# Kernel tuning notes

Hardware: AMD Instinct MI355X
Metric: run time of the kernel (lower is better)

Reference implementation:

```python
import jax, jax.numpy as jnp
import numpy as np

B, D, H, K = 16384, 128, 1024, 8
OPD = 3 * K + 1  # params per dim
TB = 3.0         # tail_bound: left=bottom=-TB, right=top=TB
EPS = 1e-12
MIN_W = MIN_H = MIN_D = 1e-3


def _masks():
    rng = np.random.RandomState(0)
    in_deg = np.arange(1, D + 1)
    h1 = rng.randint(1, D, size=(H,))
    h2 = rng.randint(1, D, size=(H,))
    out_deg = np.arange(1, D + 1)
    m1 = (in_deg[None, :] <= h1[:, None]).astype(np.float32)          # [H, D]
    m2 = (h1[None, :] <= h2[:, None]).astype(np.float32)              # [H, H]
    m3 = np.repeat((out_deg[:, None] > h2[None, :]).astype(np.float32), OPD, axis=0)  # [D*OPD, H]
    return jnp.asarray(m1), jnp.asarray(m2), jnp.asarray(m3)


def _kaiming(key, fan_out, fan_in, a=0.1):
    bound = np.sqrt(6.0 / ((1.0 + a * a) * fan_in))
    return jax.random.uniform(key, (fan_out, fan_in), jnp.float32, -bound, bound)


def setup_inputs() -> dict:
    key = jax.random.key(0)
    kx, k1, k2, k3 = jax.random.split(key, 4)
    m1, m2, m3 = _masks()
    return {
        'x': jax.random.normal(kx, (B, D), jnp.float32),
        'W1': _kaiming(k1, H, D), 'b1': jnp.zeros((H,), jnp.float32),
        'W2': _kaiming(k2, H, H), 'b2': jnp.zeros((H,), jnp.float32),
        'W3': _kaiming(k3, D * OPD, H), 'b3': jnp.zeros((D * OPD,), jnp.float32),
        'm1': m1, 'm2': m2, 'm3': m3,
    }


def _norm_cum(u, mn):
    k = u.shape[-1]
    w = jax.nn.softmax(u, axis=-1)
    w = mn + (1.0 - mn * k) * w
    c = jnp.cumsum(w, axis=-1)
    c = jnp.pad(c, [(0, 0)] * (c.ndim - 1) + [(1, 0)])
    c = c / jnp.clip(c[..., -1:], 1e-12)
    return c[..., 1:] - c[..., :-1], c


def _take(p, idx):
    return jnp.take_along_axis(p, idx[..., None], axis=-1)[..., 0]


def _forward(x, W1, b1, W2, b2, W3, b3, m1, m2, m3):
    h = jax.nn.silu(x @ (W1 * m1).T + b1)
    h = jax.nn.silu(h @ (W2 * m2).T + b2)
    raw = (h @ (W3 * m3).T + b3).reshape(-1, D, OPD)  # [B, D, 3K+1]
    uw, uh, ud = raw[..., :K], raw[..., K:2 * K], raw[..., 2 * K:]
    w, cw = _norm_cum(uw, MIN_W)
    hh, ch = _norm_cum(uh, MIN_H)
    d = MIN_D + jax.nn.softplus(ud)  # [B, D, K+1]

    left, right, bottom, top = -TB, TB, -TB, TB
    inside = (x >= left) & (x <= right)  # [B, D]
    xs = jnp.clip((x - left) / (right - left), 0.0, 1.0)
    bid = jnp.clip(jnp.sum((xs[..., None] >= cw), axis=-1) - 1, 0, K - 1)
    xk, wk = _take(cw, bid), _take(w, bid)
    yk, hk = _take(ch, bid), _take(hh, bid)
    dk, dk1 = _take(d, bid), _take(d, bid + 1)
    t = jnp.clip((xs - xk) / (wk + EPS), 0.0, 1.0)
    a = (hk + EPS) / (wk + EPS)
    num = a * t * t + dk * t * (1 - t)
    den = a + (dk + dk1 - 2 * a) * t * (1 - t)
    s = num / (den + EPS)
    y = (yk + hk * s) * (top - bottom) + bottom
    dnum = a * a * (dk1 * t * t + 2 * a * t * (1 - t) + dk * (1 - t) * (1 - t))
    dydx = (top - bottom) / (right - left) * dnum / (den * den + EPS)
    out = jnp.where(inside, y, x)
    lad = jnp.where(inside, jnp.log(jnp.clip(dydx, 1e-12)), 0.0)
    return out, jnp.sum(lad, axis=-1)


def reference(x, W1, b1, W2, b2, W3, b3, m1, m2, m3):
    return _forward(x, W1, b1, W2, b2, W3, b3, m1, m2, m3)
```

## Files before the change

### kernel.cpp

```cpp
#include <hip/hip_runtime.h>
#include <hip/hip_bf16.h>

#define BATCH 16384
#define DIM   128
#define HID   1024
#define NK    8
#define OPD   25
#define N3    (DIM*OPD)
#define NP    3328

typedef __attribute__((ext_vector_type(8))) short  short8;
typedef __attribute__((ext_vector_type(4))) float  floatx4;
typedef unsigned int u32;

__device__ __forceinline__ float fexp(float x) { return __expf(x); }
__device__ __forceinline__ float flog(float x) { return __logf(x); }
__device__ __forceinline__ float fdiv(float a, float b) { return __fdividef(a, b); }

__device__ __forceinline__ void async_copy16(const unsigned short* g,
                                             unsigned short* l) {
    __builtin_amdgcn_global_load_lds(
        (const __attribute__((address_space(1))) u32*)g,
        (__attribute__((address_space(3))) u32*)l,
        16, 0, 0);
}

__device__ __forceinline__ void swizzle_bid(int bid, int NT,
                                            int& tile, int& m) {
    const int xcd  = bid & 7;
    const int u    = bid >> 3;
    const int ph   = NT * 8;
    const int half = u / ph;
    const int rem  = u % ph;
    const int trank = rem >> 3;
    const int msub  = rem & 7;
    tile = NT - 1 - trank;
    m    = xcd * 16 + half * 8 + msub;
}

__global__ __launch_bounds__(128) void hsum_kernel(
    const float* __restrict__ m1, const float* __restrict__ m3,
    int* __restrict__ h1i, int* __restrict__ h2i) {
    const int b = blockIdx.x, t = threadIdx.x;
    if (b < HID) {
        float v = m1[b * DIM + t];
        #pragma unroll
        for (int off = 32; off > 0; off >>= 1) v += __shfl_down(v, off, 64);
        __shared__ float ws[2];
        if ((t & 63) == 0) ws[t >> 6] = v;
        __syncthreads();
        if (t == 0) h1i[b] = (int)(ws[0] + ws[1] + 0.5f);
    } else {
        const int j = (b - HID) * 128 + t;
        float s = 0.f;
        for (int d = 0; d < DIM; d++) s += m3[(size_t)d * OPD * HID + j];
        h2i[j] = DIM - (int)(s + 0.5f);
    }
}

__global__ __launch_bounds__(1024) void sort_kernel(
    const int* __restrict__ h1i, const int* __restrict__ h2i,
    int* __restrict__ perm1, int* __restrict__ perm2,
    int* __restrict__ h1sv, int* __restrict__ h2sv,
    int* __restrict__ klim1, int* __restrict__ klim2, int* __restrict__ klim3)
{
    __shared__ int hist[128];
    __shared__ int h1s[1024], h2s[1024];
    const int t = threadIdx.x;
    const int h1v = h1i[t], h2v = h2i[t];

    if (t < 128) hist[t] = 0;
    __syncthreads();
    atomicAdd(&hist[h1v], 1);
    __syncthreads();
    if (t == 0) { int a = 0; for (int b = 0; b < 128; b++) { int c = hist[b]; hist[b] = a; a += c; } }
    __syncthreads();
    int r = atomicAdd(&hist[h1v], 1);
    perm1[r] = t; h1s[r] = h1v; h1sv[r] = h1v;
    __syncthreads();
    if (t < 128) hist[t] = 0;
    __syncthreads();
    atomicAdd(&hist[h2v], 1);
    __syncthreads();
    if (t == 0) { int a = 0; for (int b = 0; b < 128; b++) { int c = hist[b]; hist[b] = a; a += c; } }
    __syncthreads();
    r = atomicAdd(&hist[h2v], 1);
    perm2[r] = t; h2s[r] = h2v; h2sv[r] = h2v;
    __syncthreads();

    if (t < 8) {
        klim1[t] = ((h1s[t * 128 + 127] + 63) >> 6) << 6;
        int mh = h2s[t * 128 + 127];
        int c = 0;
        for (int j = 0; j < 1024; j++) c += (h1s[j] <= mh) ? 1 : 0;
        klim2[t] = ((c + 63) >> 6) << 6;
    }
    if (t < 26) {
        int dmax = t * 5 + 4; if (dmax > 127) dmax = 127;
        int c = 0;
        for (int j = 0; j < 1024; j++) c += (h2s[j] <= dmax) ? 1 : 0;
        klim3[t] = ((c + 63) >> 6) << 6;
    }
}

__global__ __launch_bounds__(256) void wperm_kernel(
    const float* __restrict__ W1, const float* __restrict__ b1,
    const float* __restrict__ W2, const float* __restrict__ b2,
    const float* __restrict__ W3, const float* __restrict__ x,
    const int* __restrict__ perm1, const int* __restrict__ perm2,
    const int* __restrict__ h1sv, const int* __restrict__ h2sv,
    __hip_bfloat16* __restrict__ w1p, float* __restrict__ b1p,
    __hip_bfloat16* __restrict__ w2p, float* __restrict__ b2p,
    __hip_bfloat16* __restrict__ w3p,
    __hip_bfloat16* __restrict__ xb, float* __restrict__ lad)
{
    __shared__ float row[HID];
    const int b = blockIdx.x, t = threadIdx.x;
    if (b < 512) {
        const int i = b * 256 + t;
        const int hp = i >> 7, col = i & 127;
        const int src = perm1[hp];
        float v = (col < h1sv[hp]) ? W1[src * DIM + col] : 0.f;
        w1p[i] = __float2bfloat16(v);
        if (col == 0) b1p[hp] = b1[src];
    } else if (b < 512 + HID) {
        const int ip = b - 512;
        const int si = perm2[ip];
        const int h2v = h2sv[ip];
        #pragma unroll
        for (int q = 0; q < 4; q++) row[q * 256 + t] = W2[(size_t)si * HID + q * 256 + t];
        __syncthreads();
        #pragma unroll
        for (int q = 0; q < 4; q++) {
            const int jp = q * 256 + t;
            float v = (h1sv[jp] <= h2v) ? row[perm1[jp]] : 0.f;
            w2p[(size_t)ip * HID + jp] = __float2bfloat16(v);
        }
        if (t == 0) b2p[ip] = b2[si];
    } else if (b < 512 + HID + NP) {
        const int c = b - 512 - HID;
        const int s = c & 127, t3 = c >> 7;
        if (s >= 125) {
            #pragma unroll
            for (int q = 0; q < 4; q++)
                w3p[(size_t)c * HID + q * 256 + t] = __float2bfloat16(0.f);
            return;
        }
        const int srcrow = t3 * 125 + s;
        const int d = srcrow / 25;
        #pragma unroll
        for (int q = 0; q < 4; q++) row[q * 256 + t] = W3[(size_t)srcrow * HID + q * 256 + t];
        __syncthreads();
        #pragma unroll
        for (int q = 0; q < 4; q++) {
            const int kk = q * 256 + t;
            float v = (h2sv[kk] <= d) ? row[perm2[kk]] : 0.f;
            w3p[(size_t)c * HID + kk] = __float2bfloat16(v);
        }
    } else {
        const int i = (b - (512 + HID + NP)) * 256 + t;
        xb[i] = __float2bfloat16(x[i]);
        if (i < BATCH) lad[i] = 0.f;
    }
}

__device__ __forceinline__ void spline_eval(const float* __restrict__ p,
                                            float xv, float& yout, float& lout) {
    float cw[NK + 1], ch[NK + 1];
    {
        float mx = p[0];
        #pragma unroll
        for (int j = 1; j < NK; j++) mx = fmaxf(mx, p[j]);
        float e[NK], s = 0.f;
        #pragma unroll
        for (int j = 0; j < NK; j++) { e[j] = fexp(p[j] - mx); s += e[j]; }
        const float inv = fdiv(1.f, s);
        cw[0] = 0.f;
        #pragma unroll
        for (int j = 0; j < NK; j++) cw[j + 1] = cw[j] + (0.001f + 0.992f * e[j] * inv);
    }
    {
        float mx = p[8];
        #pragma unroll
        for (int j = 1; j < NK; j++) mx = fmaxf(mx, p[8 + j]);
        float e[NK], s = 0.f;
        #pragma unroll
        for (int j = 0; j < NK; j++) { e[j] = fexp(p[8 + j] - mx); s += e[j]; }
        const float inv = fdiv(1.f, s);
        ch[0] = 0.f;
        #pragma unroll
        for (int j = 0; j < NK; j++) ch[j + 1] = ch[j] + (0.001f + 0.992f * e[j] * inv);
    }
    const float icw = fdiv(1.f, fmaxf(cw[NK], 1e-12f));
    const float ich = fdiv(1.f, fmaxf(ch[NK], 1e-12f));

    const bool inside = (xv >= -3.f) && (xv <= 3.f);
    float xs = (xv + 3.f) * (1.f / 6.f);
    xs = fminf(fmaxf(xs, 0.f), 1.f);
    const float xsc = xs * cw[NK];

    float xk = 0.f, wk = cw[1], yk = 0.f, hk = ch[1];
    float uda = p[16], udb = p[17];
    #pragma unroll
    for (int j = 1; j < NK; j++) {
        const bool c = (xsc >= cw[j]);
        xk  = c ? cw[j] : xk;
        wk  = c ? (cw[j + 1] - cw[j]) : wk;
        yk  = c ? ch[j] : yk;
        hk  = c ? (ch[j + 1] - ch[j]) : hk;
        uda = c ? p[16 + j] : uda;
        udb = c ? p[17 + j] : udb;
    }
    xk *= icw; wk *= icw;
    yk *= ich; hk *= ich;

    const float dk  = 0.001f + ((uda > 20.f) ? uda : flog(1.f + fexp(uda)));
    const float dk1 = 0.001f + ((udb > 20.f) ? udb : flog(1.f + fexp(udb)));

    float t = fdiv(xs - xk, wk + 1e-12f);
    t = fminf(fmaxf(t, 0.f), 1.f);
    const float a   = fdiv(hk + 1e-12f, wk + 1e-12f);
    const float omt = 1.f - t;
    const float tt1 = t * omt;
    const float num = a * t * t + dk * tt1;
    const float den = a + (dk + dk1 - 2.f * a) * tt1;
    const float s   = fdiv(num, den + 1e-12f);
    const float y   = (yk + hk * s) * 6.f - 3.f;
    const float dnum = a * a * (dk1 * t * t + 2.f * a * tt1 + dk * omt * omt);
    const float dydx = fdiv(dnum, den * den + 1e-12f);

    yout = inside ? y : xv;
    lout = inside ? flog(fmaxf(dydx, 1e-12f)) : 0.f;
}

__global__ __launch_bounds__(256, 4) void gemm_bt_kernel(
    const unsigned short* __restrict__ A,
    const unsigned short* __restrict__ Bw,
    const float* __restrict__ bias,
    const int* __restrict__ klim,
    __hip_bfloat16* __restrict__ Cout,
    int M, int N, int Kd)
{
    constexpr int BM = 128, BN = 128, BK = 64;
    __shared__ unsigned short As[BM * BK];
    __shared__ unsigned short Bs[BN * BK];

    const int bid = blockIdx.y * gridDim.x + blockIdx.x;
    int tile, mpan;
    swizzle_bid(bid, gridDim.x, tile, mpan);
    const int bn = tile * BN;
    const int bm = mpan * BM;
    const int Klim = klim[tile];

    const int t    = threadIdx.x;
    const int lane = t & 63;
    const int w    = t >> 6;
    const int wr   = (w >> 1) * 64;
    const int wc   = (w & 1) * 64;
    const int lr   = lane & 15;
    const int quad = lane >> 4;
    const int lxor = lr & 7;

    floatx4 acc[4][4] = {};

    const int lrow = lane >> 3;
    const int lcol = ((lane & 7) ^ lrow) * 8;

    for (int k0 = 0; k0 < Klim; k0 += BK) {
        __syncthreads();
        #pragma unroll
        for (int p = 0; p < 4; p++) {
            const int q = w * 4 + p;
            const int r = q * 8 + lrow;
            async_copy16(&A[(size_t)(bm + r) * Kd + k0 + lcol],
                         &As[q * 512 + lane * 8]);
            async_copy16(&Bw[(size_t)(bn + r) * Kd + k0 + lcol],
                         &Bs[q * 512 + lane * 8]);
        }
        __syncthreads();
        #pragma unroll
        for (int ks = 0; ks < BK; ks += 32) {
            const int cbase = (ks >> 3) + quad;
            const int coff  = (cbase ^ lxor) * 8;
            short8 af[4], bfr[4];
            #pragma unroll
            for (int i = 0; i < 4; i++)
                af[i] = *(const short8*)&As[(wr + i * 16 + lr) * BK + coff];
            #pragma unroll
            for (int j = 0; j < 4; j++)
                bfr[j] = *(const short8*)&Bs[(wc + j * 16 + lr) * BK + coff];
            #pragma unroll
            for (int i = 0; i < 4; i++)
                #pragma unroll
                for (int j = 0; j < 4; j++)
                    acc[i][j] = __builtin_amdgcn_mfma_f32_16x16x32_bf16(
                        af[i], bfr[j], acc[i][j], 0, 0, 0);
        }
    }

    #pragma unroll
    for (int j = 0; j < 4; j++) {
        const int col = bn + wc + j * 16 + lr;
        const float bv = bias[col];
        #pragma unroll
        for (int i = 0; i < 4; i++) {
            const int rowb = bm + wr + i * 16 + quad * 4;
            #pragma unroll
            for (int r = 0; r < 4; r++) {
                float v = acc[i][j][r] + bv;
                v = v * fdiv(1.f, 1.f + fexp(-v));
                Cout[(size_t)(rowb + r) * N + col] = __float2bfloat16(v);
            }
        }
    }
}

__global__ __launch_bounds__(256, 4) void gemm3_spline_kernel(
    const unsigned short* __restrict__ A,
    const unsigned short* __restrict__ Bw,
    const float* __restrict__ b3,
    const int* __restrict__ klim,
    const float* __restrict__ x,
    float* __restrict__ out,
    float* __restrict__ lad,
    int M)
{
    constexpr int BM = 128, BN = 128, BK = 64, Kd = HID;
    constexpr int GS = 28;
    constexpr int RS = 140;
    __shared__ __align__(16) char smem[64 * RS * 4 + 128 * 4];
    unsigned short* As = (unsigned short*)smem;
    unsigned short* Bs = (unsigned short*)(smem + BM * BK * 2);
    float* eb     = (float*)smem;
    float* ladacc = (float*)(smem + 64 * RS * 4);

    const int bid = blockIdx.y * gridDim.x + blockIdx.x;
    int tile, mpan;
    swizzle_bid(bid, gridDim.x, tile, mpan);
    const int bn = tile * BN;
    const int bm = mpan * BM;
    const int Klim = klim[tile];

    const int t    = threadIdx.x;
    const int lane = t & 63;
    const int w    = t >> 6;
    const int wr   = (w >> 1) * 64;
    const int wc   = (w & 1) * 64;
    const int lr   = lane & 15;
    const int quad = lane >> 4;
    const int lxor = lr & 7;

    if (t < 128) ladacc[t] = 0.f;

    floatx4 acc[4][4] = {};

    const int lrow = lane >> 3;
    const int lcol = ((lane & 7) ^ lrow) * 8;

    for (int k0 = 0; k0 < Klim; k0 += BK) {
        __syncthreads();
        #pragma unroll
        for (int p = 0; p < 4; p++) {
            const int q = w * 4 + p;
            const int r = q * 8 + lrow;
            async_copy16(&A[(size_t)(bm + r) * Kd + k0 + lcol],
                         &As[q * 512 + lane * 8]);
            async_copy16(&Bw[(size_t)(bn + r) * Kd + k0 + lcol],
                         &Bs[q * 512 + lane * 8]);
        }
        __syncthreads();
        #pragma unroll
        for (int ks = 0; ks < BK; ks += 32) {
            const int cbase = (ks >> 3) + quad;
            const int coff  = (cbase ^ lxor) * 8;
            short8 af[4], bfr[4];
            #pragma unroll
            for (int i = 0; i < 4; i++)
                af[i] = *(const short8*)&As[(wr + i * 16 + lr) * BK + coff];
            #pragma unroll
            for (int j = 0; j < 4; j++)
                bfr[j] = *(const short8*)&Bs[(wc + j * 16 + lr) * BK + coff];
            #pragma unroll
            for (int i = 0; i < 4; i++)
                #pragma unroll
                for (int j = 0; j < 4; j++)
                    acc[i][j] = __builtin_amdgcn_mfma_f32_16x16x32_bf16(
                        af[i], bfr[j], acc[i][j], 0, 0, 0);
        }
    }

    #pragma unroll 1
    for (int h = 0; h < 2; h++) {
        __syncthreads();
        if ((w >> 1) == h) {
            #pragma unroll
            for (int j = 0; j < 4; j++) {
                const int s = wc + j * 16 + lr;
                if (s < 125) {
                    const int grp = s / 25, within = s % 25;
                    const int off = grp * GS + within;
                    const int bidx = tile * 125 + s;
                    const float bv = b3[bidx < N3 ? bidx : 0];
                    #pragma unroll
                    for (int i = 0; i < 4; i++) {
                        const int lrw = i * 16 + quad * 4;
                        #pragma unroll
                        for (int r2 = 0; r2 < 4; r2++)
                            eb[(lrw + r2) * RS + off] = acc[i][j][r2] + bv;
                    }
                }
            }
        }
        __syncthreads();
        #pragma unroll 1
        for (int q = t; q < 320; q += 256) {
            const int r  = q / 5;
            const int ds = q % 5;
            const int dim = tile * 5 + ds;
            if (dim < DIM) {
                float pl[28];
                const floatx4* pv = (const floatx4*)(eb + r * RS + ds * GS);
                #pragma unroll
                for (int ii = 0; ii < 7; ii++) ((floatx4*)pl)[ii] = pv[ii];
                const int grow = bm + h * 64 + r;
                const float xv = x[(size_t)grow * DIM + dim];
                float y, l;
                spline_eval(pl, xv, y, l);
                out[(size_t)grow * DIM + dim] = y;
                atomicAdd(&ladacc[h * 64 + r], l);
            }
        }
    }
    __syncthreads();
    if (t < 128) atomicAdd(&lad[bm + t], ladacc[t]);
}

extern "C" void kernel_launch(void* const* d_in, const int* in_sizes, int n_in,
                              void* d_out, int out_size, void* d_ws, size_t ws_size,
                              hipStream_t stream) {
    const float* x  = (const float*)d_in[0];
    const float* W1 = (const float*)d_in[1];
    const float* b1 = (const float*)d_in[2];
    const float* W2 = (const float*)d_in[3];
    const float* b2 = (const float*)d_in[4];
    const float* W3 = (const float*)d_in[5];
    const float* b3 = (const float*)d_in[6];
    const float* m1 = (const float*)d_in[7];
    const float* m3 = (const float*)d_in[9];

    char* ws = (char*)d_ws;
    const size_t OFF_W1B = 0;
    const size_t OFF_W2B = OFF_W1B + (size_t)HID * DIM * 2;
    const size_t OFF_W3P = OFF_W2B + (size_t)HID * HID * 2;
    const size_t OFF_XB  = OFF_W3P + (size_t)NP * HID * 2;
    const size_t OFF_H1B = OFF_XB  + (size_t)BATCH * DIM * 2;
    const size_t OFF_H2B = OFF_H1B + (size_t)BATCH * HID * 2;
    const size_t OFF_SML = OFF_H2B + (size_t)BATCH * HID * 2;

    __hip_bfloat16* w1p = (__hip_bfloat16*)(ws + OFF_W1B);
    __hip_bfloat16* w2p = (__hip_bfloat16*)(ws + OFF_W2B);
    __hip_bfloat16* w3p = (__hip_bfloat16*)(ws + OFF_W3P);
    __hip_bfloat16* xb  = (__hip_bfloat16*)(ws + OFF_XB);
    __hip_bfloat16* h1b = (__hip_bfloat16*)(ws + OFF_H1B);
    __hip_bfloat16* h2b = (__hip_bfloat16*)(ws + OFF_H2B);

    float* b1p   = (float*)(ws + OFF_SML);
    float* b2p   = b1p + HID;
    int*   h1i   = (int*)(b2p + HID);
    int*   h2i   = h1i + HID;
    int*   perm1 = h2i + HID;
    int*   perm2 = perm1 + HID;
    int*   h1sv  = perm2 + HID;
    int*   h2sv  = h1sv + HID;
    int*   klim1 = h2sv + HID;
    int*   klim2 = klim1 + 8;
    int*   klim3 = klim2 + 8;

    float* out_p = (float*)d_out;
    float* lad_p = out_p + (size_t)BATCH * DIM;

    hsum_kernel<<<HID + 8, 128, 0, stream>>>(m1, m3, h1i, h2i);
    sort_kernel<<<1, 1024, 0, stream>>>(h1i, h2i, perm1, perm2, h1sv, h2sv,
                                        klim1, klim2, klim3);
    wperm_kernel<<<512 + HID + NP + (BATCH * DIM) / 256, 256, 0, stream>>>(
        W1, b1, W2, b2, W3, x, perm1, perm2, h1sv, h2sv,
        w1p, b1p, w2p, b2p, w3p, xb, lad_p);

    gemm_bt_kernel<<<dim3(HID / 128, BATCH / 128), 256, 0, stream>>>(
        (const unsigned short*)xb, (const unsigned short*)w1p, b1p, klim1, h1b,
        BATCH, HID, DIM);
    gemm_bt_kernel<<<dim3(HID / 128, BATCH / 128), 256, 0, stream>>>(
        (const unsigned short*)h1b, (const unsigned short*)w2p, b2p, klim2, h2b,
        BATCH, HID, HID);
    gemm3_spline_kernel<<<dim3(NP / 128, BATCH / 128), 256, 0, stream>>>(
        (const unsigned short*)h2b, (const unsigned short*)w3p, b3, klim3, x,
        out_p, lad_p, BATCH);
}
```

Before: 268.2 us.

## Merge mask reduction into sort kernel and prefetch x into LDS for spline

Merges the mask-sum kernel into the single-block sort kernel, which now also converts x to bf16 and zeroes lad in its extra blocks, so one launch and one dependency hop are removed. The wperm kernel no longer carries the x-conversion blocks. In the fused GEMM3+spline kernel, the x values each tile needs are fetched asynchronously into LDS at kernel start, replacing the scattered global loads in the spline epilogue. The cost is a single 1024-thread block doing serial mask sums, which could lengthen the critical path, plus extra LDS per block in the GEMM kernel that may affect occupancy.

```diff
diff --git a/kernel.cpp b/kernel.cpp
--- a/kernel.cpp
+++ b/kernel.cpp
@@ -23,6 +23,12 @@
         (const __attribute__((address_space(1))) u32*)g,
         (__attribute__((address_space(3))) u32*)l,
         16, 0, 0);
+}
+__device__ __forceinline__ void async_copy4(const float* g, float* l) {
+    __builtin_amdgcn_global_load_lds(
+        (const __attribute__((address_space(1))) u32*)g,
+        (__attribute__((address_space(3))) u32*)l,
+        4, 0, 0);
 }
 
 __device__ __forceinline__ void swizzle_bid(int bid, int NT,
@@ -38,36 +44,39 @@
     m    = xcd * 16 + half * 8 + msub;
 }
 
-__global__ __launch_bounds__(128) void hsum_kernel(
+__global__ __launch_bounds__(1024) void prep0_kernel(
     const float* __restrict__ m1, const float* __restrict__ m3,
-    int* __restrict__ h1i, int* __restrict__ h2i) {
-    const int b = blockIdx.x, t = threadIdx.x;
-    if (b < HID) {
-        float v = m1[b * DIM + t];
-        #pragma unroll
-        for (int off = 32; off > 0; off >>= 1) v += __shfl_down(v, off, 64);
-        __shared__ float ws[2];
-        if ((t & 63) == 0) ws[t >> 6] = v;
-        __syncthreads();
-        if (t == 0) h1i[b] = (int)(ws[0] + ws[1] + 0.5f);
-    } else {
-        const int j = (b - HID) * 128 + t;
-        float s = 0.f;
-        for (int d = 0; d < DIM; d++) s += m3[(size_t)d * OPD * HID + j];
-        h2i[j] = DIM - (int)(s + 0.5f);
-    }
-}
-
-__global__ __launch_bounds__(1024) void sort_kernel(
-    const int* __restrict__ h1i, const int* __restrict__ h2i,
+    const float* __restrict__ x,
+    __hip_bfloat16* __restrict__ xb, float* __restrict__ lad,
     int* __restrict__ perm1, int* __restrict__ perm2,
     int* __restrict__ h1sv, int* __restrict__ h2sv,
     int* __restrict__ klim1, int* __restrict__ klim2, int* __restrict__ klim3)
 {
+    if (blockIdx.x > 0) {
+        const int i = (blockIdx.x - 1) * 1024 + threadIdx.x;
+        xb[i] = __float2bfloat16(x[i]);
+        if (i < BATCH) lad[i] = 0.f;
+        return;
+    }
     __shared__ int hist[128];
     __shared__ int h1s[1024], h2s[1024];
+    __shared__ int h1loc[1024], h2loc[1024];
     const int t = threadIdx.x;
-    const int h1v = h1i[t], h2v = h2i[t];
+
+    {
+        float s = 0.f;
+        const float4* r = (const float4*)(m1 + (size_t)t * DIM);
+        #pragma unroll
+        for (int q = 0; q < 32; q++) { float4 v = r[q]; s += v.x + v.y + v.z + v.w; }
+        h1loc[t] = (int)(s + 0.5f);
+    }
+    {
+        float s = 0.f;
+        for (int d = 0; d < DIM; d++) s += m3[(size_t)d * OPD * HID + t];
+        h2loc[t] = DIM - (int)(s + 0.5f);
+    }
+    __syncthreads();
+    const int h1v = h1loc[t], h2v = h2loc[t];
 
     if (t < 128) hist[t] = 0;
     __syncthreads();
@@ -106,13 +115,12 @@
 __global__ __launch_bounds__(256) void wperm_kernel(
     const float* __restrict__ W1, const float* __restrict__ b1,
     const float* __restrict__ W2, const float* __restrict__ b2,
-    const float* __restrict__ W3, const float* __restrict__ x,
+    const float* __restrict__ W3,
     const int* __restrict__ perm1, const int* __restrict__ perm2,
     const int* __restrict__ h1sv, const int* __restrict__ h2sv,
     __hip_bfloat16* __restrict__ w1p, float* __restrict__ b1p,
     __hip_bfloat16* __restrict__ w2p, float* __restrict__ b2p,
-    __hip_bfloat16* __restrict__ w3p,
-    __hip_bfloat16* __restrict__ xb, float* __restrict__ lad)
+    __hip_bfloat16* __restrict__ w3p)
 {
     __shared__ float row[HID];
     const int b = blockIdx.x, t = threadIdx.x;
@@ -137,7 +145,7 @@
             w2p[(size_t)ip * HID + jp] = __float2bfloat16(v);
         }
         if (t == 0) b2p[ip] = b2[si];
-    } else if (b < 512 + HID + NP) {
+    } else {
         const int c = b - 512 - HID;
         const int s = c & 127, t3 = c >> 7;
         if (s >= 125) {
@@ -157,10 +165,6 @@
             float v = (h2sv[kk] <= d) ? row[perm2[kk]] : 0.f;
             w3p[(size_t)c * HID + kk] = __float2bfloat16(v);
         }
-    } else {
-        const int i = (b - (512 + HID + NP)) * 256 + t;
-        xb[i] = __float2bfloat16(x[i]);
-        if (i < BATCH) lad[i] = 0.f;
     }
 }
 
@@ -328,11 +332,12 @@
     constexpr int BM = 128, BN = 128, BK = 64, Kd = HID;
     constexpr int GS = 28;
     constexpr int RS = 140;
-    __shared__ __align__(16) char smem[64 * RS * 4 + 128 * 4];
+    __shared__ __align__(16) char smem[64 * RS * 4 + 128 * 4 + 640 * 4];
     unsigned short* As = (unsigned short*)smem;
     unsigned short* Bs = (unsigned short*)(smem + BM * BK * 2);
     float* eb     = (float*)smem;
     float* ladacc = (float*)(smem + 64 * RS * 4);
+    float* xls    = (float*)(smem + 64 * RS * 4 + 128 * 4);
 
     const int bid = blockIdx.y * gridDim.x + blockIdx.x;
     int tile, mpan;
@@ -351,6 +356,16 @@
     const int lxor = lr & 7;
 
     if (t < 128) ladacc[t] = 0.f;
+
+    #pragma unroll
+    for (int ii = 0; ii < 3; ii++) {
+        const int q = t + ii * 256;
+        if (q < 640) {
+            const int r = q / 5, ds = q % 5;
+            int dim = tile * 5 + ds; if (dim >= DIM) dim = 0;
+            async_copy4(&x[(size_t)(bm + r) * DIM + dim], &xls[q]);
+        }
+    }
 
     floatx4 acc[4][4] = {};
 
@@ -423,7 +438,7 @@
                 #pragma unroll
                 for (int ii = 0; ii < 7; ii++) ((floatx4*)pl)[ii] = pv[ii];
                 const int grow = bm + h * 64 + r;
-                const float xv = x[(size_t)grow * DIM + dim];
+                const float xv = xls[(h * 64 + r) * 5 + ds];
                 float y, l;
                 spline_eval(pl, xv, y, l);
                 out[(size_t)grow * DIM + dim] = y;
@@ -479,12 +494,11 @@
     float* out_p = (float*)d_out;
     float* lad_p = out_p + (size_t)BATCH * DIM;
 
-    hsum_kernel<<<HID + 8, 128, 0, stream>>>(m1, m3, h1i, h2i);
-    sort_kernel<<<1, 1024, 0, stream>>>(h1i, h2i, perm1, perm2, h1sv, h2sv,
-                                        klim1, klim2, klim3);
-    wperm_kernel<<<512 + HID + NP + (BATCH * DIM) / 256, 256, 0, stream>>>(
-        W1, b1, W2, b2, W3, x, perm1, perm2, h1sv, h2sv,
-        w1p, b1p, w2p, b2p, w3p, xb, lad_p);
+    prep0_kernel<<<1 + (BATCH * DIM) / 1024, 1024, 0, stream>>>(
+        m1, m3, x, xb, lad_p, perm1, perm2, h1sv, h2sv, klim1, klim2, klim3);
+    wperm_kernel<<<512 + HID + NP, 256, 0, stream>>>(
+        W1, b1, W2, b2, W3, perm1, perm2, h1sv, h2sv,
+        w1p, b1p, w2p, b2p, w3p);
 
     gemm_bt_kernel<<<dim3(HID / 128, BATCH / 128), 256, 0, stream>>>(
         (const unsigned short*)xb, (const unsigned short*)w1p, b1p, klim1, h1b,
```

After: 275.8 us. 1.03x slower.
